# Kernel optimization log

Hardware: AMD Instinct MI355X
Metric: run time of the kernel (lower is better)

The kernel has to match this reference:

```python
import jax, jax.numpy as jnp
import numpy as np

B, L, DC, DQ, H = 32, 1024, 1024, 1024, 512
NEG_NUM = -10000.0


def setup_inputs() -> dict:
    key = jax.random.key(0)
    ks = jax.random.split(key, 7)
    s1 = 1.0 / np.sqrt(DC + DQ)
    s2 = 1.0 / np.sqrt(H)
    return {
        "ctx": jax.random.normal(ks[0], (B, L, DC), jnp.float32),
        "query": jax.random.normal(ks[1], (B, DQ), jnp.float32),
        "mask": jnp.ones((B, L), jnp.int32),
        "noise": jax.random.normal(ks[2], (B, L), jnp.float32),
        "W1": jax.random.uniform(ks[3], (DC + DQ, H), jnp.float32, -s1, s1),
        "b1": jax.random.uniform(ks[4], (H,), jnp.float32, -s1, s1),
        "w2": jax.random.uniform(ks[5], (H,), jnp.float32, -s2, s2),
        "b2": jnp.zeros((), jnp.float32),
    }


def reference(ctx, query, mask, noise, W1, b1, w2, b2):
    b, l, dc = ctx.shape
    # concat([ctx, query_expanded]) @ W1 == ctx @ W1[:DC] + query @ W1[DC:]
    hidden = jnp.tanh(
        jnp.einsum("blc,ch->blh", ctx, W1[:dc])
        + (query @ W1[dc:])[:, None, :]
        + b1
    )  # [B, L, H]
    score = hidden @ w2 + b2  # [B, L]
    score = jnp.where(mask == 0, NEG_NUM, score)
    score = score + noise  # sigmoid_noise=True -> coefficient 1
    p = jax.nn.sigmoid(score)  # p_choose_i [B, L]

    # initial prev_att: one-hot at position 0
    prev_att = jnp.zeros((b, l), score.dtype).at[:, 0].set(1.0)
    # shifted (1 - p): [1, 1-p_0, ..., 1-p_{L-2}]
    shifted = jnp.concatenate(
        [jnp.ones((b, 1), p.dtype), 1.0 - p[:, :-1]], axis=1
    )

    # linear recurrence a_t = shifted_t * a_{t-1} + prev_att_t  (a_{-1}=0)
    def step(carry, xs):
        s_t, pr_t = xs
        a = s_t * carry + pr_t
        return a, a

    _, att_t = jax.lax.scan(step, jnp.zeros((b,), p.dtype), (shifted.T, prev_att.T))
    att = att_t.T * p  # [B, L]

    expected_ctx = jnp.einsum("bl,blc->bc", att, ctx)  # bmm(p_ctx[:,None,:], ctx)
    return expected_ctx, att
```

## Files before the change

### kernel.cpp

```cpp
#include <hip/hip_runtime.h>
#include <hip/hip_bf16.h>
#include <math.h>

constexpr int Bb = 32;
constexpr int Ll = 1024;
constexpr int DC = 1024;
constexpr int DQ = 1024;
constexpr int Hh = 512;
#define NEG_NUM -10000.0f

typedef __attribute__((ext_vector_type(8))) short bf16x8;
typedef __attribute__((ext_vector_type(4))) float f32x4;

#define GLOAD_LDS16(g, l)                                                  \
    __builtin_amdgcn_global_load_lds(                                      \
        (const __attribute__((address_space(1))) void*)(g),                \
        (__attribute__((address_space(3))) void*)(l), 16, 0, 0)

__device__ inline unsigned short f2bf(float f) {
    unsigned int x = __float_as_uint(f);
    unsigned int r = (x + 0x7FFFu + ((x >> 16) & 1u)) >> 16;
    return (unsigned short)r;
}
__device__ inline float bfu(unsigned short u) {
    return __uint_as_float(((unsigned int)u) << 16);
}


__global__ __launch_bounds__(256) void prep_kernel(const float* __restrict__ W1,
                                                   const float* __restrict__ query,
                                                   const float* __restrict__ b1,
                                                   unsigned short* __restrict__ w1t,
                                                   float* __restrict__ qb,
                                                   float* __restrict__ score,
                                                   float* __restrict__ out_ctx) {
    __shared__ float red[4][64];
    const int bid = blockIdx.x;
    if (bid < 2048) {
        int idx = bid * 256 + threadIdx.x;
        int n = idx >> 10, k = idx & 1023;
        int ks = k ^ ((n & 7) << 3);
        w1t[(size_t)n * 1024 + ks] = f2bf(W1[(size_t)k * Hh + n]);
    } else if (bid < 2176) {
        int i = (bid - 2048) * 256 + threadIdx.x;
        out_ctx[i] = 0.f;
        score[i] = 0.f;
    } else {
        const int qbid = bid - 2176;
        const int b  = qbid >> 3;
        const int hg = qbid & 7;
        const int hl = threadIdx.x & 63;
        const int j  = threadIdx.x >> 6;
        const int h  = hg * 64 + hl;
        const float* q = query + (size_t)b * DQ + j * 256;
        const float* w = W1 + (size_t)(DC + j * 256) * Hh + h;
        float a0 = 0.f, a1 = 0.f, a2 = 0.f, a3 = 0.f;
#pragma unroll 4
        for (int c = 0; c < 256; c += 4) {
            a0 += q[c + 0] * w[(size_t)(c + 0) * Hh];
            a1 += q[c + 1] * w[(size_t)(c + 1) * Hh];
            a2 += q[c + 2] * w[(size_t)(c + 2) * Hh];
            a3 += q[c + 3] * w[(size_t)(c + 3) * Hh];
        }
        red[j][hl] = (a0 + a1) + (a2 + a3);
        __syncthreads();
        if (j == 0)
            qb[(size_t)b * Hh + h] = red[0][hl] + red[1][hl] + red[2][hl] + red[3][hl] + b1[h];
    }
}

__global__ __launch_bounds__(256) void cvt_ctx_kernel(const float* __restrict__ in,
                                                      unsigned short* __restrict__ out) {
    size_t i = (size_t)(blockIdx.x * 256 + threadIdx.x) * 8;
    int row = (int)(i >> 10);
    int col = (int)(i & 1023);
    float4 v0 = *(const float4*)(in + i);
    float4 v1 = *(const float4*)(in + i + 4);
    union { unsigned short us[8]; uint4 v; } o;
    o.us[0] = f2bf(v0.x); o.us[1] = f2bf(v0.y); o.us[2] = f2bf(v0.z); o.us[3] = f2bf(v0.w);
    o.us[4] = f2bf(v1.x); o.us[5] = f2bf(v1.y); o.us[6] = f2bf(v1.z); o.us[7] = f2bf(v1.w);
    *(uint4*)(out + ((size_t)row << 10) + (col ^ ((row & 7) << 3))) = o.v;
}

__global__ __launch_bounds__(256) void gemm_mfma(const unsigned short* __restrict__ ctxb,
                                                 const unsigned short* __restrict__ w1t,
                                                 const float* __restrict__ qb,
                                                 const float* __restrict__ w2,
                                                 float* __restrict__ score) {
    __shared__ unsigned short As[128 * 64];
    __shared__ unsigned short Bs[128 * 64];

    const int m0 = blockIdx.x * 128;
    const int n0 = blockIdx.y * 128;
    const int tid = threadIdx.x;
    const int w = tid >> 6, lane = tid & 63;
    const int wr = w >> 1, wc = w & 1;
    const int lr = lane & 15, lk = lane >> 4;

    const char* ctxB = (const char*)ctxb;
    const char* w1tB = (const char*)w1t;
    char* AsB = (char*)As;
    char* BsB = (char*)Bs;

    const int srow = tid >> 3;
    const int scolb = (tid & 7) * 16;

    const int x = (lr & 7) << 4;

    f32x4 acc[4][4];
#pragma unroll
    for (int mf = 0; mf < 4; ++mf)
#pragma unroll
        for (int nf = 0; nf < 4; ++nf) acc[mf][nf] = (f32x4){0.f, 0.f, 0.f, 0.f};

    for (int k0 = 0; k0 < DC; k0 += 64) {
#pragma unroll
        for (int i = 0; i < 4; ++i) {
            int row = i * 32 + srow;
            GLOAD_LDS16(ctxB + (size_t)(m0 + row) * 2048 + k0 * 2 + scolb,
                        AsB + i * 4096 + tid * 16);
            GLOAD_LDS16(w1tB + (size_t)(n0 + row) * 2048 + k0 * 2 + scolb,
                        BsB + i * 4096 + tid * 16);
        }
        __syncthreads();

#pragma unroll
        for (int kk = 0; kk < 2; ++kk) {
            const int colb = (kk * 64 + lk * 16) ^ x;
            bf16x8 a[4], bb[4];
#pragma unroll
            for (int mf = 0; mf < 4; ++mf)
                a[mf] = *(const bf16x8*)(AsB + (wr * 64 + mf * 16 + lr) * 128 + colb);
#pragma unroll
            for (int nf = 0; nf < 4; ++nf)
                bb[nf] = *(const bf16x8*)(BsB + (wc * 64 + nf * 16 + lr) * 128 + colb);
#pragma unroll
            for (int mf = 0; mf < 4; ++mf)
#pragma unroll
                for (int nf = 0; nf < 4; ++nf)
                    acc[mf][nf] = __builtin_amdgcn_mfma_f32_16x16x32_bf16(a[mf], bb[nf], acc[mf][nf], 0, 0, 0);
        }
        __syncthreads();
    }

    const int bq = m0 >> 10;
    const float* qbb = qb + (size_t)bq * Hh;
#pragma unroll
    for (int mf = 0; mf < 4; ++mf) {
        float s0 = 0.f, s1 = 0.f, s2 = 0.f, s3 = 0.f;
#pragma unroll
        for (int nf = 0; nf < 4; ++nf) {
            int col = n0 + wc * 64 + nf * 16 + lr;
            float wv = w2[col];
            float qv = qbb[col];
            s0 += tanhf(acc[mf][nf][0] + qv) * wv;
            s1 += tanhf(acc[mf][nf][1] + qv) * wv;
            s2 += tanhf(acc[mf][nf][2] + qv) * wv;
            s3 += tanhf(acc[mf][nf][3] + qv) * wv;
        }
#pragma unroll
        for (int off = 8; off; off >>= 1) {
            s0 += __shfl_xor(s0, off, 16);
            s1 += __shfl_xor(s1, off, 16);
            s2 += __shfl_xor(s2, off, 16);
            s3 += __shfl_xor(s3, off, 16);
        }
        if (lr == 0) {
            int row = m0 + wr * 64 + mf * 16 + lk * 4;
            atomicAdd(&score[row + 0], s0);
            atomicAdd(&score[row + 1], s1);
            atomicAdd(&score[row + 2], s2);
            atomicAdd(&score[row + 3], s3);
        }
    }
}

__global__ __launch_bounds__(64) void scan_kernel(const float* __restrict__ score,
                                                  const int* __restrict__ mask,
                                                  const float* __restrict__ noise,
                                                  const float* __restrict__ b2p,
                                                  float* __restrict__ att) {
    int b = blockIdx.x;
    int lane = threadIdx.x;
    float b2 = b2p[0];
    int base = b * Ll + lane * 16;

    float p[16], q[16];
    float run = 1.f;
#pragma unroll
    for (int j = 0; j < 16; ++j) {
        int l = base + j;
        float s = score[l] + b2;
        if (mask[l] == 0) s = NEG_NUM;
        s += noise[l];
        float pv = 1.f / (1.f + expf(-s));
        p[j] = pv;
        run *= (1.f - pv);
        q[j] = run;
    }
    float incl = run;
#pragma unroll
    for (int off = 1; off < 64; off <<= 1) {
        float v = __shfl_up(incl, off, 64);
        if (lane >= off) incl *= v;
    }
    float excl = __shfl_up(incl, 1, 64);
    if (lane == 0) excl = 1.f;
#pragma unroll
    for (int j = 0; j < 16; ++j) {
        float P = excl * (j == 0 ? 1.f : q[j - 1]);
        att[base + j] = p[j] * P;
    }
}

__global__ __launch_bounds__(256) void ectx_bf16_kernel(const unsigned short* __restrict__ ctxb,
                                                        const float* __restrict__ att,
                                                        float* __restrict__ out) {
    int b = blockIdx.z;
    int c4 = threadIdx.x;
    int l0 = blockIdx.y * 128;
    const unsigned short* cb = ctxb + ((size_t)b * Ll + l0) * DC;
    const float* ab = att + (size_t)b * Ll + l0;
    const int c = c4 * 4;
    float a0 = 0.f, a1 = 0.f, a2 = 0.f, a3 = 0.f;
    for (int l = 0; l < 128; ++l) {
        float av = ab[l];
        int cs = c ^ ((l & 7) << 3);
        ushort4 v = *(const ushort4*)(cb + (size_t)l * DC + cs);
        a0 += av * bfu(v.x); a1 += av * bfu(v.y);
        a2 += av * bfu(v.z); a3 += av * bfu(v.w);
    }
    float* o = out + (size_t)b * DC + c;
    atomicAdd(o + 0, a0); atomicAdd(o + 1, a1);
    atomicAdd(o + 2, a2); atomicAdd(o + 3, a3);
}

extern "C" void kernel_launch(void* const* d_in, const int* in_sizes, int n_in,
                              void* d_out, int out_size, void* d_ws, size_t ws_size,
                              hipStream_t stream) {
    const float* ctx   = (const float*)d_in[0];
    const float* query = (const float*)d_in[1];
    const int*   mask  = (const int*)d_in[2];
    const float* noise = (const float*)d_in[3];
    const float* W1    = (const float*)d_in[4];
    const float* b1    = (const float*)d_in[5];
    const float* w2    = (const float*)d_in[6];
    const float* b2    = (const float*)d_in[7];

    float* out_ctx = (float*)d_out;
    float* out_att = (float*)d_out + Bb * DC;

    char* ws = (char*)d_ws;
    float* score = (float*)ws;
    float* qb    = (float*)(ws + 131072);
    unsigned short* w1t  = (unsigned short*)(ws + 196608);
    unsigned short* ctxb = (unsigned short*)(ws + 1245184);

    prep_kernel<<<2432, 256, 0, stream>>>(W1, query, b1, w1t, qb, score, out_ctx);

    cvt_ctx_kernel<<<(Bb * Ll * DC) / (256 * 8), 256, 0, stream>>>(ctx, ctxb);

    gemm_mfma<<<dim3((Bb * Ll) / 128, Hh / 128), 256, 0, stream>>>(ctxb, w1t, qb, w2, score);

    scan_kernel<<<Bb, 64, 0, stream>>>(score, mask, noise, b2, out_att);

    ectx_bf16_kernel<<<dim3(1, Ll / 128, Bb), 256, 0, stream>>>(ctxb, out_att, out_ctx);
}
```

Baseline: 123.5 us.

## Fold ctx conversion into prep kernel and switch GEMM to intra-block split-K

The ctx fp32→bf16 conversion moves into the prep kernel as extra blocks, which removes one kernel launch. The GEMM becomes 64x64 tiles in which each of the four waves handles its own quarter of K with a private LDS region and no block-level barriers in the K loop. Partial accumulators are reduced through LDS before the tanh/w2 epilogue. The smaller tiles load A and B more times in total and use 64KB of LDS per block, which may limit occupancy. In exchange the per-wave pipelines run independently.

```diff
diff --git a/kernel.cpp b/kernel.cpp
--- a/kernel.cpp
+++ b/kernel.cpp
@@ -30,10 +30,12 @@
 __global__ __launch_bounds__(256) void prep_kernel(const float* __restrict__ W1,
                                                    const float* __restrict__ query,
                                                    const float* __restrict__ b1,
+                                                   const float* __restrict__ ctx,
                                                    unsigned short* __restrict__ w1t,
                                                    float* __restrict__ qb,
                                                    float* __restrict__ score,
-                                                   float* __restrict__ out_ctx) {
+                                                   float* __restrict__ out_ctx,
+                                                   unsigned short* __restrict__ ctxb) {
     __shared__ float red[4][64];
     const int bid = blockIdx.x;
     if (bid < 2048) {
@@ -45,7 +47,7 @@
         int i = (bid - 2048) * 256 + threadIdx.x;
         out_ctx[i] = 0.f;
         score[i] = 0.f;
-    } else {
+    } else if (bid < 2432) {
         const int qbid = bid - 2176;
         const int b  = qbid >> 3;
         const int hg = qbid & 7;
@@ -66,45 +68,38 @@
         __syncthreads();
         if (j == 0)
             qb[(size_t)b * Hh + h] = red[0][hl] + red[1][hl] + red[2][hl] + red[3][hl] + b1[h];
-    }
-}
-
-__global__ __launch_bounds__(256) void cvt_ctx_kernel(const float* __restrict__ in,
-                                                      unsigned short* __restrict__ out) {
-    size_t i = (size_t)(blockIdx.x * 256 + threadIdx.x) * 8;
-    int row = (int)(i >> 10);
-    int col = (int)(i & 1023);
-    float4 v0 = *(const float4*)(in + i);
-    float4 v1 = *(const float4*)(in + i + 4);
-    union { unsigned short us[8]; uint4 v; } o;
-    o.us[0] = f2bf(v0.x); o.us[1] = f2bf(v0.y); o.us[2] = f2bf(v0.z); o.us[3] = f2bf(v0.w);
-    o.us[4] = f2bf(v1.x); o.us[5] = f2bf(v1.y); o.us[6] = f2bf(v1.z); o.us[7] = f2bf(v1.w);
-    *(uint4*)(out + ((size_t)row << 10) + (col ^ ((row & 7) << 3))) = o.v;
-}
-
-__global__ __launch_bounds__(256) void gemm_mfma(const unsigned short* __restrict__ ctxb,
-                                                 const unsigned short* __restrict__ w1t,
-                                                 const float* __restrict__ qb,
-                                                 const float* __restrict__ w2,
-                                                 float* __restrict__ score) {
-    __shared__ unsigned short As[128 * 64];
-    __shared__ unsigned short Bs[128 * 64];
-
-    const int m0 = blockIdx.x * 128;
-    const int n0 = blockIdx.y * 128;
+    } else {
+        size_t i = (size_t)((bid - 2432) * 256 + threadIdx.x) * 8;
+        int row = (int)(i >> 10);
+        int col = (int)(i & 1023);
+        float4 v0 = *(const float4*)(ctx + i);
+        float4 v1 = *(const float4*)(ctx + i + 4);
+        union { unsigned short us[8]; uint4 v; } o;
+        o.us[0] = f2bf(v0.x); o.us[1] = f2bf(v0.y); o.us[2] = f2bf(v0.z); o.us[3] = f2bf(v0.w);
+        o.us[4] = f2bf(v1.x); o.us[5] = f2bf(v1.y); o.us[6] = f2bf(v1.z); o.us[7] = f2bf(v1.w);
+        *(uint4*)(ctxb + ((size_t)row << 10) + (col ^ ((row & 7) << 3))) = o.v;
+    }
+}
+
+__global__ __launch_bounds__(256) void gemm_splitk(const unsigned short* __restrict__ ctxb,
+                                                   const unsigned short* __restrict__ w1t,
+                                                   const float* __restrict__ qb,
+                                                   const float* __restrict__ w2,
+                                                   float* __restrict__ score) {
+    __shared__ char lds[4 * 16384];
+
+    const int n0 = blockIdx.x * 64;
+    const int m0 = blockIdx.y * 64;
     const int tid = threadIdx.x;
-    const int w = tid >> 6, lane = tid & 63;
-    const int wr = w >> 1, wc = w & 1;
+    const int wv = tid >> 6, lane = tid & 63;
     const int lr = lane & 15, lk = lane >> 4;
 
+    char* base = lds + wv * 16384;
     const char* ctxB = (const char*)ctxb;
     const char* w1tB = (const char*)w1t;
-    char* AsB = (char*)As;
-    char* BsB = (char*)Bs;
-
-    const int srow = tid >> 3;
-    const int scolb = (tid & 7) * 16;
-
+
+    const int srow = lane >> 3;
+    const int scolb = (lane & 7) * 16;
     const int x = (lr & 7) << 4;
 
     f32x4 acc[4][4];
@@ -113,65 +108,73 @@
 #pragma unroll
         for (int nf = 0; nf < 4; ++nf) acc[mf][nf] = (f32x4){0.f, 0.f, 0.f, 0.f};
 
-    for (int k0 = 0; k0 < DC; k0 += 64) {
-#pragma unroll
-        for (int i = 0; i < 4; ++i) {
-            int row = i * 32 + srow;
+    for (int c = 0; c < 4; ++c) {
+        const int k0 = wv * 256 + c * 64;
+        __builtin_amdgcn_sched_barrier(0);
+#pragma unroll
+        for (int i = 0; i < 8; ++i) {
+            int row = i * 8 + srow;
             GLOAD_LDS16(ctxB + (size_t)(m0 + row) * 2048 + k0 * 2 + scolb,
-                        AsB + i * 4096 + tid * 16);
+                        base + i * 1024 + lane * 16);
             GLOAD_LDS16(w1tB + (size_t)(n0 + row) * 2048 + k0 * 2 + scolb,
-                        BsB + i * 4096 + tid * 16);
+                        base + 8192 + i * 1024 + lane * 16);
         }
-        __syncthreads();
-
+        asm volatile("s_waitcnt vmcnt(0)" ::: "memory");
+        __builtin_amdgcn_sched_barrier(0);
 #pragma unroll
         for (int kk = 0; kk < 2; ++kk) {
             const int colb = (kk * 64 + lk * 16) ^ x;
             bf16x8 a[4], bb[4];
 #pragma unroll
             for (int mf = 0; mf < 4; ++mf)
-                a[mf] = *(const bf16x8*)(AsB + (wr * 64 + mf * 16 + lr) * 128 + colb);
+                a[mf] = *(const bf16x8*)(base + (mf * 16 + lr) * 128 + colb);
 #pragma unroll
             for (int nf = 0; nf < 4; ++nf)
-                bb[nf] = *(const bf16x8*)(BsB + (wc * 64 + nf * 16 + lr) * 128 + colb);
+                bb[nf] = *(const bf16x8*)(base + 8192 + (nf * 16 + lr) * 128 + colb);
 #pragma unroll
             for (int mf = 0; mf < 4; ++mf)
 #pragma unroll
                 for (int nf = 0; nf < 4; ++nf)
                     acc[mf][nf] = __builtin_amdgcn_mfma_f32_16x16x32_bf16(a[mf], bb[nf], acc[mf][nf], 0, 0, 0);
         }
-        __syncthreads();
-    }
-
-    const int bq = m0 >> 10;
-    const float* qbb = qb + (size_t)bq * Hh;
-#pragma unroll
-    for (int mf = 0; mf < 4; ++mf) {
-        float s0 = 0.f, s1 = 0.f, s2 = 0.f, s3 = 0.f;
-#pragma unroll
-        for (int nf = 0; nf < 4; ++nf) {
-            int col = n0 + wc * 64 + nf * 16 + lr;
-            float wv = w2[col];
-            float qv = qbb[col];
-            s0 += tanhf(acc[mf][nf][0] + qv) * wv;
-            s1 += tanhf(acc[mf][nf][1] + qv) * wv;
-            s2 += tanhf(acc[mf][nf][2] + qv) * wv;
-            s3 += tanhf(acc[mf][nf][3] + qv) * wv;
-        }
-#pragma unroll
-        for (int off = 8; off; off >>= 1) {
-            s0 += __shfl_xor(s0, off, 16);
-            s1 += __shfl_xor(s1, off, 16);
-            s2 += __shfl_xor(s2, off, 16);
-            s3 += __shfl_xor(s3, off, 16);
-        }
-        if (lr == 0) {
-            int row = m0 + wr * 64 + mf * 16 + lk * 4;
-            atomicAdd(&score[row + 0], s0);
-            atomicAdd(&score[row + 1], s1);
-            atomicAdd(&score[row + 2], s2);
-            atomicAdd(&score[row + 3], s3);
-        }
+    }
+
+#pragma unroll
+    for (int mf = 0; mf < 4; ++mf)
+#pragma unroll
+        for (int nf = 0; nf < 4; ++nf)
+            *(f32x4*)(base + (mf * 4 + nf) * 1024 + lane * 16) = acc[mf][nf];
+    __syncthreads();
+
+    const float* qbb = qb + (size_t)(m0 >> 10) * Hh;
+    float s0 = 0.f, s1 = 0.f, s2 = 0.f, s3 = 0.f;
+#pragma unroll
+    for (int nf = 0; nf < 4; ++nf) {
+        f32x4 t = (f32x4){0.f, 0.f, 0.f, 0.f};
+#pragma unroll
+        for (int w = 0; w < 4; ++w)
+            t += *(const f32x4*)(lds + w * 16384 + (wv * 4 + nf) * 1024 + lane * 16);
+        int col = n0 + nf * 16 + lr;
+        float wvw = w2[col];
+        float qv = qbb[col];
+        s0 += tanhf(t[0] + qv) * wvw;
+        s1 += tanhf(t[1] + qv) * wvw;
+        s2 += tanhf(t[2] + qv) * wvw;
+        s3 += tanhf(t[3] + qv) * wvw;
+    }
+#pragma unroll
+    for (int off = 8; off; off >>= 1) {
+        s0 += __shfl_xor(s0, off, 16);
+        s1 += __shfl_xor(s1, off, 16);
+        s2 += __shfl_xor(s2, off, 16);
+        s3 += __shfl_xor(s3, off, 16);
+    }
+    if (lr == 0) {
+        int row = m0 + wv * 16 + lk * 4;
+        atomicAdd(&score[row + 0], s0);
+        atomicAdd(&score[row + 1], s1);
+        atomicAdd(&score[row + 2], s2);
+        atomicAdd(&score[row + 3], s3);
     }
 }
 
@@ -256,11 +259,9 @@
     unsigned short* w1t  = (unsigned short*)(ws + 196608);
     unsigned short* ctxb = (unsigned short*)(ws + 1245184);
 
-    prep_kernel<<<2432, 256, 0, stream>>>(W1, query, b1, w1t, qb, score, out_ctx);
-
-    cvt_ctx_kernel<<<(Bb * Ll * DC) / (256 * 8), 256, 0, stream>>>(ctx, ctxb);
-
-    gemm_mfma<<<dim3((Bb * Ll) / 128, Hh / 128), 256, 0, stream>>>(ctxb, w1t, qb, w2, score);
+    prep_kernel<<<18816, 256, 0, stream>>>(W1, query, b1, ctx, w1t, qb, score, out_ctx, ctxb);
+
+    gemm_splitk<<<dim3(Hh / 64, (Bb * Ll) / 64), 256, 0, stream>>>(ctxb, w1t, qb, w2, score);
 
     scan_kernel<<<Bb, 64, 0, stream>>>(score, mask, noise, b2, out_att);
 
```

After: 142.5 us. 15.4% more time.
